# Optimization experiments

Hardware: AMD Instinct MI355X
Metric: run time of the kernel (lower is better)

## Reference

```python
import jax, jax.numpy as jnp
import numpy as np

B, T, H, W, C = 2, 8, 20, 36, 512
NH = 4
HD = C // NH
WS = (5, 9)
EXP = (2, 4)              # window_size // 2
KP = (5, 9)               # focal unfold kernel for level k=0
PADP = (2, 4)
T2T_K, T2T_S, T2T_P = (7, 7), (3, 3), (3, 3)
FFN_HD = 1960
NWH, NWW = H // WS[0], W // WS[1]   # 4, 4
WAREA = WS[0] * WS[1]               # 45


def _valid_ind_rolled():
    wh, ww = WS
    eh, ew = EXP
    m = np.ones((4, wh, ww), np.float32)
    m[0, :wh - eh, :ww - ew] = 0   # tl
    m[1, :wh - eh, ew:] = 0        # tr
    m[2, eh:, :ww - ew] = 0        # bl
    m[3, eh:, ew:] = 0             # br
    return jnp.asarray(np.nonzero(m.reshape(-1))[0])

VALID_ROLLED = _valid_ind_rolled()  # (120,)


def unfold(x, k, s, p):
    # x: (N, Cc, Hh, Ww) -> (N, Cc*kh*kw, L); matches torch.nn.Unfold layout (c slowest).
    N, Cc, Hh, Ww = x.shape
    kh, kw = k; sh, sw = s; ph, pw = p
    xp = jnp.pad(x, ((0, 0), (0, 0), (ph, ph), (pw, pw)))
    oh = (Hh + 2 * ph - kh) // sh + 1
    ow = (Ww + 2 * pw - kw) // sw + 1
    cols = [xp[:, :, i:i + oh * sh:sh, j:j + ow * sw:sw]
            for i in range(kh) for j in range(kw)]
    patches = jnp.stack(cols, axis=2)            # (N, Cc, kh*kw, oh, ow)
    return patches.reshape(N, Cc * kh * kw, oh * ow)


def fold(patches, out_hw, k, s, p):
    # inverse of unfold (overlap-add), matches torch F.fold.
    N = patches.shape[0]
    kh, kw = k; sh, sw = s; ph, pw = p
    Hh, Ww = out_hw
    oh = (Hh + 2 * ph - kh) // sh + 1
    ow = (Ww + 2 * pw - kw) // sw + 1
    Cc = patches.shape[1] // (kh * kw)
    pr = patches.reshape(N, Cc, kh, kw, oh, ow)
    out = jnp.zeros((N, Cc, Hh + 2 * ph, Ww + 2 * pw), patches.dtype)
    for i in range(kh):
        for j in range(kw):
            out = out.at[:, :, i:i + oh * sh:sh, j:j + ow * sw:sw].add(pr[:, :, i, j])
    return out[:, :, ph:ph + Hh, pw:pw + Ww]


def layer_norm(x, g, b):
    mu = jnp.mean(x, -1, keepdims=True)
    var = jnp.var(x, -1, keepdims=True)
    return (x - mu) * jax.lax.rsqrt(var + 1e-5) * g + b


def win_part(x):
    # (B,T,H,W,C) -> (B*nW, T*wh*ww, C)
    b = x.shape[0]
    x = x.reshape(b, T, NWH, WS[0], NWW, WS[1], C)
    return x.transpose(0, 2, 4, 1, 3, 5, 6).reshape(-1, T * WAREA, C)


def to_heads(w):
    return w.reshape(-1, T, WAREA, NH, HD).transpose(0, 3, 1, 2, 4).reshape(-1, NH, T * WAREA, HD)


def block_forward(x, g1, be1, wqkv, bqkv, wproj, bproj, wpool, bpool, g2, be2, w1, bf1, w2, bf2, out_h, out_w):
    shortcut = x
    xn = layer_norm(x, g1, be1)

    # ---- coarser (pooled) focal level, k=0 (focal_level=2) ----
    wnr = xn.reshape(B, T, NWH, WS[0], NWW, WS[1], C).transpose(0, 2, 4, 1, 3, 5, 6)
    wnr = wnr.reshape(B, NWH, NWW, T, WAREA, C)
    pooled = jnp.einsum('bhwtnc,n->bhwtc', wnr, wpool) + bpool   # (B,NWH,NWW,T,C)

    # ---- window attention ----
    qkv = xn @ wqkv + bqkv                                       # (B,T,H,W,3C)
    q, k, v = jnp.split(qkv, 3, axis=-1)
    qw = to_heads(win_part(q)) * (HD ** -0.5)
    kw_, vw = to_heads(win_part(k)), to_heads(win_part(v))

    def rolled(t):
        parts = []
        for sh, sw in ((-EXP[0], -EXP[1]), (-EXP[0], EXP[1]), (EXP[0], -EXP[1]), (EXP[0], EXP[1])):
            r = jnp.roll(t, (sh, sw), axis=(2, 3))
            parts.append(win_part(r).reshape(-1, T, WAREA, NH, HD))
        cat = jnp.concatenate(parts, axis=2)                     # (B*nW, T, 4*warea, NH, HD)
        cat = jnp.take(cat.transpose(0, 3, 1, 2, 4), VALID_ROLLED, axis=3)
        return cat.reshape(-1, NH, T * VALID_ROLLED.shape[0], HD)

    k_rolled = jnp.concatenate([kw_, rolled(k)], axis=2)         # (B*nW, NH, T*165, HD)
    v_rolled = jnp.concatenate([vw, rolled(v)], axis=2)

    # pooled keys/values via focal unfold
    xp = pooled.transpose(0, 3, 1, 2, 4)                          # (B,T,NWH,NWW,C)
    qkv_p = xp @ wqkv + bqkv
    kp, vp = qkv_p[..., C:2 * C], qkv_p[..., 2 * C:]

    def unfold_kv(t):
        t = t.transpose(0, 1, 4, 2, 3).reshape(B * T, C, NWH, NWW)
        u = unfold(t, KP, (1, 1), PADP)                           # (B*T, C*45, L)
        L = u.shape[-1]
        u = u.reshape(B, T, C, KP[0], KP[1], L).transpose(0, 5, 1, 3, 4, 2)
        u = u.reshape(B * L, T, KP[0] * KP[1], NH, HD).transpose(0, 3, 1, 2, 4)
        return u.reshape(B * L, NH, T * KP[0] * KP[1], HD)

    k_all = jnp.concatenate([k_rolled, unfold_kv(kp)], axis=2)
    v_all = jnp.concatenate([v_rolled, unfold_kv(vp)], axis=2)

    attn = jnp.einsum('wnqd,wnkd->wnqk', qw, k_all)               # (B*nW, NH, T*45, N)

    # validity mask for pooled context (zero-padded unfold positions -> -100)
    ones = jnp.ones((T, 1, NWH, NWW), x.dtype)
    um = unfold(ones, KP, (1, 1), PADP)                           # (T, 45, L)
    L = um.shape[-1]
    mvals = jnp.where(um.reshape(T, KP[0] * KP[1], L).transpose(2, 0, 1).reshape(L, -1) == 0,
                      jnp.asarray(-100.0, x.dtype), jnp.asarray(0.0, x.dtype))
    n_rolled = k_rolled.shape[2]
    mask_cols = jnp.concatenate([jnp.zeros((L, n_rolled), x.dtype), mvals], axis=1)
    attn = attn + jnp.tile(mask_cols, (B, 1))[:, None, None, :]

    attn = jax.nn.softmax(attn, axis=-1)
    out = jnp.einsum('wnqk,wnkd->wnqd', attn, v_all)
    out = out.transpose(0, 2, 1, 3).reshape(-1, T * WAREA, C) @ wproj + bproj

    # window reverse + residual
    out = out.reshape(B, NWH, NWW, T, WS[0], WS[1], C)
    out = out.transpose(0, 3, 1, 4, 2, 5, 6).reshape(B, T, H, W, C)
    x = shortcut + out

    # ---- FusionFeedForward (fold/unfold re-normalized MLP) ----
    y = layer_norm(x, g2, be2).reshape(B, T * H * W, C)
    h = y @ w1 + bf1                                              # (B, n, 1960)
    nvec = ((out_h + 2 * T2T_P[0] - T2T_K[0]) // T2T_S[0] + 1) * \
           ((out_w + 2 * T2T_P[1] - T2T_K[1]) // T2T_S[1] + 1)
    bt = (B * T * H * W) // nvec
    norm_p = jnp.ones((bt, T2T_K[0] * T2T_K[1], nvec), x.dtype)
    norm_f = fold(norm_p, (out_h, out_w), T2T_K, T2T_S, T2T_P)    # (bt,1,out_h,out_w)
    h_f = fold(h.reshape(bt, nvec, FFN_HD).transpose(0, 2, 1), (out_h, out_w), T2T_K, T2T_S, T2T_P)
    h = unfold(h_f / norm_f, T2T_K, T2T_S, T2T_P).transpose(0, 2, 1).reshape(B, T * H * W, FFN_HD)
    h = jax.nn.gelu(h, approximate=False) @ w2 + bf2
    return x + h.reshape(B, T, H, W, C)


def setup_inputs() -> dict:
    key = jax.random.key(0)
    ks = jax.random.split(key, 8)
    s = 0.02
    return dict(
        x=jax.random.normal(ks[0], (B, T, H, W, C), jnp.float32),
        g1=jnp.ones((C,), jnp.float32),
        be1=jnp.zeros((C,), jnp.float32),
        wqkv=jax.random.normal(ks[1], (C, 3 * C), jnp.float32) * s,
        bqkv=jnp.zeros((3 * C,), jnp.float32),
        wproj=jax.random.normal(ks[2], (C, C), jnp.float32) * s,
        bproj=jnp.zeros((C,), jnp.float32),
        wpool=jnp.full((WAREA,), 1.0 / WAREA, jnp.float32),
        bpool=jnp.zeros((1,), jnp.float32),
        g2=jnp.ones((C,), jnp.float32),
        be2=jnp.zeros((C,), jnp.float32),
        w1=jax.random.normal(ks[3], (C, FFN_HD), jnp.float32) * s,
        bf1=jnp.zeros((FFN_HD,), jnp.float32),
        w2=jax.random.normal(ks[4], (FFN_HD, C), jnp.float32) * s,
        bf2=jnp.zeros((C,), jnp.float32),
        out_h=60,
        out_w=108,
    )


def reference(x, g1, be1, wqkv, bqkv, wproj, bproj, wpool, bpool, g2, be2, w1, bf1, w2, bf2, out_h, out_w):
    return block_forward(x, g1, be1, wqkv, bqkv, wproj, bproj, wpool, bpool,
                         g2, be2, w1, bf1, w2, bf2, out_h, out_w)
```

## Files before the change

### kernel.cpp

```cpp
#include <hip/hip_runtime.h>
#include <hip/hip_bf16.h>
#include <math.h>

typedef __hip_bfloat16 bf16;
typedef __attribute__((ext_vector_type(8))) short bf16x8;
typedef __attribute__((ext_vector_type(4))) float f32x4;

#define DEVI __device__ __forceinline__

#define C_ 512
#define NH_ 4
#define NTOK 11520
#define NKEY 1680
#define NRK 120
#define FFN_ 1960
#define ZROW (NTOK + 256)

DEVI float ldf(const bf16* p) { return __bfloat162float(*p); }
DEVI float ldf(const float* p) { return *p; }
DEVI void stw(bf16* p, float v) { *p = __float2bfloat16(v); }
DEVI void stw(float* p, float v) { *p = v; }
DEVI unsigned short f2bs(float f) { bf16 h = __float2bfloat16(f); return *(unsigned short*)&h; }

template <int DT> DEVI float ldw(const void* p, size_t i) {
  if (DT == 0) return __bfloat162float(((const bf16*)p)[i]);
  else         return ((const float*)p)[i];
}

DEVI void gload_lds16(const void* g, void* l) {
  __builtin_amdgcn_global_load_lds(
      (const __attribute__((address_space(1))) void*)g,
      (__attribute__((address_space(3))) void*)l, 16, 0, 0);
}

__global__ void k_init(const void* __restrict__ g1, int* __restrict__ flag,
                       int* __restrict__ table, bf16* __restrict__ zp) {
  if (blockIdx.x == 0) {
    if (threadIdx.x == 0) {
      const unsigned short* p = (const unsigned short*)g1;
      *flag = (p[0] == 0x3F80u) ? 0 : 1;
      int cnt = 0;
      for (int pq = 0; pq < 4; pq++)
        for (int wi = 0; wi < 5; wi++)
          for (int wj = 0; wj < 9; wj++) {
            bool invalid;
            if (pq == 0)      invalid = (wi < 3) && (wj < 5);
            else if (pq == 1) invalid = (wi < 3) && (wj >= 4);
            else if (pq == 2) invalid = (wi >= 2) && (wj < 5);
            else              invalid = (wi >= 2) && (wj >= 4);
            if (!invalid) table[cnt++] = pq * 45 + wi * 9 + wj;
          }
    }
  } else {
    zp[(blockIdx.x - 1) * 256 + threadIdx.x] = __float2bfloat16(0.f);
  }
}

__global__ void k_ksrc(const int* __restrict__ vtab, int* __restrict__ ksrc) {
  int idx = blockIdx.x * 256 + threadIdx.x;
  if (idx >= 32 * NKEY) return;
  int w = idx / NKEY, j = idx % NKEY;
  int b = w >> 4, nh = (w >> 2) & 3, nw = w & 3;
  int val;
  if (j < 360) {
    int t = j / 45, pos = j % 45, wi = pos / 9, wj2 = pos % 9;
    val = ((b * 8 + t) * 20 + nh * 5 + wi) * 36 + nw * 9 + wj2;
  } else if (j < 1320) {
    int jj = j - 360;
    int t = jj / 120, r = jj % 120;
    int id = vtab[r];
    int p = id / 45, pos = id % 45, wi = pos / 9, wj2 = pos % 9;
    int sh = (p < 2) ? -2 : 2;
    int sw = (p & 1) ? 4 : -4;
    int hh = nh * 5 + wi - sh;
    if (hh < 0) hh += 20; else if (hh >= 20) hh -= 20;
    int ww2 = nw * 9 + wj2 - sw;
    if (ww2 < 0) ww2 += 36; else if (ww2 >= 36) ww2 -= 36;
    val = ((b * 8 + t) * 20 + hh) * 36 + ww2;
  } else {
    int jj = j - 1320;
    int t = jj / 45, kidx = jj % 45, ki = kidx / 9, kj = kidx % 9;
    int snh = nh + ki - 2, snw = nw + kj - 4;
    if (snh < 0 || snh >= 4 || snw < 0 || snw >= 4) val = -1;
    else val = NTOK + (b * 8 + t) * 16 + snh * 4 + snw;
  }
  ksrc[idx] = val;
}

template <int DT>
DEVI void wcvt_body(const void* in, bf16* out, int K, int N, int Npad) {
  __shared__ float t[64][65];
  const int n0 = blockIdx.x * 64;
  const int k0 = blockIdx.y * 64;
  const int tx = threadIdx.x & 63, tg = threadIdx.x >> 6;
#pragma unroll
  for (int r = 0; r < 16; r++) {
    int k = k0 + r * 4 + tg;
    int nn = n0 + tx;
    float v = (k < K && nn < N) ? ldw<DT>(in, (size_t)k * N + nn) : 0.f;
    t[r * 4 + tg][tx] = v;
  }
  __syncthreads();
#pragma unroll
  for (int r = 0; r < 16; r++) {
    int nn = n0 + r * 4 + tg;
    int k = k0 + tx;
    if (nn < Npad && k < K)
      out[(size_t)nn * K + k] = __float2bfloat16(t[tx][r * 4 + tg]);
  }
}
__global__ void k_wcvt(const int* __restrict__ dflag, const void* __restrict__ in,
                       bf16* __restrict__ out, int K, int N, int Npad) {
  if (*dflag == 0) wcvt_body<0>(in, out, K, N, Npad);
  else             wcvt_body<1>(in, out, K, N, Npad);
}

__global__ void k_bcvt4(const int* __restrict__ dflag,
                        const void* __restrict__ b0, float* __restrict__ o0,
                        const void* __restrict__ b1, float* __restrict__ o1,
                        const void* __restrict__ b2, float* __restrict__ o2,
                        const void* __restrict__ b3, float* __restrict__ o3) {
  int dt = *dflag;
  int bx = blockIdx.x;
  const void* src; float* dst; int n, i;
  if (bx < 6)       { src = b0; dst = o0; n = 1536; i = bx * 256 + threadIdx.x; }
  else if (bx < 8)  { src = b1; dst = o1; n = 512;  i = (bx - 6) * 256 + threadIdx.x; }
  else if (bx < 16) { src = b2; dst = o2; n = FFN_; i = (bx - 8) * 256 + threadIdx.x; }
  else              { src = b3; dst = o3; n = 512;  i = (bx - 16) * 256 + threadIdx.x; }
  if (i < n) dst[i] = (dt == 0) ? ldw<0>(src, i) : ldw<1>(src, i);
}

template <int DTIN, int DTP>
DEVI void ln_body(const void* xin, const void* g, const void* be, bf16* out) {
  const int tok = blockIdx.x;
  const int tid = threadIdx.x;
  const size_t base = (size_t)tok * C_;
  float v0 = ldw<DTIN>(xin, base + tid);
  float v1 = ldw<DTIN>(xin, base + tid + 256);
  float s = v0 + v1, ss = v0 * v0 + v1 * v1;
#pragma unroll
  for (int o = 32; o; o >>= 1) { s += __shfl_xor(s, o); ss += __shfl_xor(ss, o); }
  __shared__ float sh[10];
  const int lane = tid & 63, wv = tid >> 6;
  if (lane == 0) { sh[wv] = s; sh[4 + wv] = ss; }
  __syncthreads();
  if (tid == 0) {
    float a = sh[0] + sh[1] + sh[2] + sh[3];
    float q = sh[4] + sh[5] + sh[6] + sh[7];
    float mu = a * (1.0f / C_);
    float var = q * (1.0f / C_) - mu * mu;
    sh[8] = mu; sh[9] = rsqrtf(fmaxf(var, 0.f) + 1e-5f);
  }
  __syncthreads();
  float mu = sh[8], inv = sh[9];
  stw(out + base + tid,
      (v0 - mu) * inv * ldw<DTP>(g, tid) + ldw<DTP>(be, tid));
  stw(out + base + tid + 256,
      (v1 - mu) * inv * ldw<DTP>(g, tid + 256) + ldw<DTP>(be, tid + 256));
}
__global__ void k_ln(const int* __restrict__ dflag, int mode,
                     const void* __restrict__ xin, const void* __restrict__ g,
                     const void* __restrict__ be, bf16* __restrict__ out) {
  int dt = *dflag;
  if (mode == 0) {
    if (dt == 0) ln_body<0, 0>(xin, g, be, out);
    else         ln_body<1, 1>(xin, g, be, out);
  } else {
    if (dt == 0) ln_body<1, 0>(xin, g, be, out);
    else         ln_body<1, 1>(xin, g, be, out);
  }
}

template <int DT>
DEVI void pool_body(const bf16* xn, const void* wpool, const void* bpool,
                    float* pooled) {
  int idx = blockIdx.x * blockDim.x + threadIdx.x;
  if (idx >= 256 * C_) return;
  int c = idx & (C_ - 1);
  int fw = idx >> 9;
  int nw = fw & 3, nh = (fw >> 2) & 3;
  int bt = fw >> 4;
  float acc = ldw<DT>(bpool, 0);
  for (int wi = 0; wi < 5; wi++) {
    int hh = nh * 5 + wi;
    const bf16* base = xn + (((size_t)(bt * 20 + hh)) * 36 + nw * 9) * C_ + c;
    for (int wj = 0; wj < 9; wj++)
      acc += __bfloat162float(base[(size_t)wj * C_]) * ldw<DT>(wpool, wi * 9 + wj);
  }
  pooled[idx] = acc;
}
__global__ void k_pool(const int* __restrict__ dflag, const bf16* __restrict__ xn,
                       const void* __restrict__ wpool, const void* __restrict__ bpool,
                       float* __restrict__ pooled) {
  if (*dflag == 0) pool_body<0>(xn, wpool, bpool, pooled);
  else             pool_body<1>(xn, wpool, bpool, pooled);
}

template <int DT>
DEVI void gemm_small_body(const float* A, const void* Bw, const void* bias,
                          bf16* Cc) {
  __shared__ float As[8][512];
  const int n = blockIdx.x * 256 + threadIdx.x;
  const int m0 = blockIdx.y * 8;
  for (int i = threadIdx.x; i < 8 * 512; i += 256)
    As[i >> 9][i & 511] = A[(size_t)(m0 + (i >> 9)) * 512 + (i & 511)];
  __syncthreads();
  float acc[8];
  float bv = ldw<DT>(bias, n);
#pragma unroll
  for (int mm = 0; mm < 8; mm++) acc[mm] = bv;
  for (int k = 0; k < 512; k++) {
    float b = ldw<DT>(Bw, (size_t)k * 1536 + n);
#pragma unroll
    for (int mm = 0; mm < 8; mm++) acc[mm] += As[mm][k] * b;
  }
#pragma unroll
  for (int mm = 0; mm < 8; mm++)
    Cc[(size_t)(m0 + mm) * 1536 + n] = __float2bfloat16(acc[mm]);
}
__global__ void k_gemm_small(const int* __restrict__ dflag, const float* __restrict__ A,
                             const void* __restrict__ Bw, const void* __restrict__ bias,
                             bf16* __restrict__ Cc) {
  if (*dflag == 0) gemm_small_body<0>(A, Bw, bias, Cc);
  else             gemm_small_body<1>(A, Bw, bias, Cc);
}

template <int RES>
__global__ __launch_bounds__(256) void k_gemm_m(const int* __restrict__ dflag,
                                                const bf16* __restrict__ A,
                                                const bf16* __restrict__ Bt,
                                                const float* __restrict__ bias,
                                                const void* __restrict__ resid,
                                                void* __restrict__ out,
                                                int M, int N, int K) {
  const int dt = dflag ? *dflag : 0;
  __shared__ __align__(16) unsigned short As[2][128 * 32];
  __shared__ __align__(16) unsigned short Bs[2][128 * 32];
  const int tid = threadIdx.x;
  const int lane = tid & 63, wid = tid >> 6;
  const int r15 = lane & 15, quad = lane >> 4;
  const int wm = wid >> 1, wn = wid & 1;
  const int nbx = gridDim.x;
  const int lin = blockIdx.x + nbx * blockIdx.y;
  const int cpx = (nbx * gridDim.y) >> 3;
  const int swz = (lin & 7) * cpx + (lin >> 3);
  const int m0 = (swz / nbx) * 128, n0 = (swz % nbx) * 128;

  f32x4 acc[4][4];
#pragma unroll
  for (int i = 0; i < 4; i++)
#pragma unroll
    for (int j = 0; j < 4; j++)
#pragma unroll
      for (int e = 0; e < 4; e++) acc[i][j][e] = 0.f;

  const int lrow = lane >> 2, lcol = (lane & 3) * 8;

  for (int k0 = 0; k0 < K; k0 += 64) {
    int rem = K - k0;
    if (rem >= 64) {
      const bf16* ga = A + (size_t)(m0 + wid * 32 + lrow) * K + k0 + lcol;
      gload_lds16(ga, &As[0][wid * 1024]);
      gload_lds16(ga + (size_t)16 * K, &As[0][wid * 1024 + 512]);
      gload_lds16(ga + 32, &As[1][wid * 1024]);
      gload_lds16(ga + (size_t)16 * K + 32, &As[1][wid * 1024 + 512]);
      const bf16* gb = Bt + (size_t)(n0 + wid * 32 + lrow) * K + k0 + lcol;
      gload_lds16(gb, &Bs[0][wid * 1024]);
      gload_lds16(gb + (size_t)16 * K, &Bs[0][wid * 1024 + 512]);
      gload_lds16(gb + 32, &Bs[1][wid * 1024]);
      gload_lds16(gb + (size_t)16 * K + 32, &Bs[1][wid * 1024 + 512]);
    } else {
      int r = tid >> 3, c = (tid & 7) * 8;
      uint4 z = make_uint4(0, 0, 0, 0);
      int h = c >> 5, cc = c & 31;
#pragma unroll
      for (int p = 0; p < 4; p++) {
        int row = r + p * 32;
        uint4 av = z, bv = z;
        if (c < rem) {
          av = *(const uint4*)(A + (size_t)(m0 + row) * K + k0 + c);
          bv = *(const uint4*)(Bt + (size_t)(n0 + row) * K + k0 + c);
        }
        *(uint4*)&As[h][row * 32 + cc] = av;
        *(uint4*)&Bs[h][row * 32 + cc] = bv;
      }
    }
    __syncthreads();

#pragma unroll
    for (int h = 0; h < 2; h++) {
      bf16x8 af[4], bfr[4];
#pragma unroll
      for (int mf = 0; mf < 4; mf++)
        af[mf] = *(const bf16x8*)&As[h][(wm * 64 + mf * 16 + r15) * 32 + quad * 8];
#pragma unroll
      for (int nf = 0; nf < 4; nf++)
        bfr[nf] = *(const bf16x8*)&Bs[h][(wn * 64 + nf * 16 + r15) * 32 + quad * 8];
#pragma unroll
      for (int mf = 0; mf < 4; mf++)
#pragma unroll
        for (int nf = 0; nf < 4; nf++)
          acc[mf][nf] = __builtin_amdgcn_mfma_f32_16x16x32_bf16(af[mf], bfr[nf],
                                                                acc[mf][nf], 0, 0, 0);
    }
    __syncthreads();
  }

#pragma unroll
  for (int nf = 0; nf < 4; nf++) {
    int n = n0 + wn * 64 + nf * 16 + r15;
    if (n >= N) continue;
    float bv = bias[n];
#pragma unroll
    for (int mf = 0; mf < 4; mf++) {
      int mb = m0 + wm * 64 + mf * 16 + quad * 4;
#pragma unroll
      for (int e = 0; e < 4; e++) {
        size_t off = (size_t)(mb + e) * N + n;
        float v = acc[mf][nf][e] + bv;
        if (RES == 1) v += (dt == 0) ? ldw<0>(resid, off) : ldw<1>(resid, off);
        else if (RES == 2) v += ((const float*)resid)[off];
        if (RES == 0) ((bf16*)out)[off] = __float2bfloat16(v);
        else if (RES == 1) ((float*)out)[off] = v;
        else {
          if (dt == 0) ((bf16*)out)[off] = __float2bfloat16(v);
          else         ((float*)out)[off] = v;
        }
      }
    }
  }
}

#define KT 64
#define KPAD 136
#define VPAD 72
__global__ __launch_bounds__(768) void k_attn_m(const bf16* __restrict__ qkv,
                                                const int* __restrict__ ksrc,
                                                bf16* __restrict__ ao) {
  __shared__ int ks_l[NKEY];
  __shared__ __align__(16) unsigned short ktl[2][KT * KPAD];
  __shared__ __align__(16) unsigned short vtl[2][128 * VPAD];
  __shared__ __align__(16) unsigned short ptl[12 * 16 * VPAD];
  __shared__ float maskv[2][KT];

  const int tid = threadIdx.x;
  const int lane = tid & 63, wid = tid >> 6;
  const int r15 = lane & 15, quad = lane >> 4;
  const int w = blockIdx.x, qt = blockIdx.y, n = blockIdx.z;
  const int b = w >> 4, nh = (w >> 2) & 3, nw = w & 3;
  const unsigned short* qkvs = (const unsigned short*)qkv;

  for (int j = tid; j < NKEY; j += 768) ks_l[j] = ksrc[w * NKEY + j];

  bf16x8 qf[4];
  {
    int qw = qt * 192 + wid * 16 + r15;
    int qc2 = qw < 360 ? qw : 359;
    int t = qc2 / 45, pos = qc2 % 45, wi = pos / 9, wj = pos % 9;
    int tok = ((b * 8 + t) * 20 + nh * 5 + wi) * 36 + nw * 9 + wj;
    const unsigned short* qp = qkvs + (size_t)tok * 1536 + n * 128 + quad * 8;
#pragma unroll
    for (int c = 0; c < 4; c++)
      qf[c] = *(const bf16x8*)(qp + c * 32);
  }

  f32x4 of[8];
#pragma unroll
  for (int nt = 0; nt < 8; nt++)
#pragma unroll
    for (int e = 0; e < 4; e++) of[nt][e] = 0.f;
  float m_[4], l_[4];
#pragma unroll
  for (int e = 0; e < 4; e++) { m_[e] = -1e30f; l_[e] = 0.f; }

  unsigned short* ptw = &ptl[wid * 16 * VPAD];

  const bool isK = (wid < 4);
  const int kr = tid >> 2, kp = tid & 3;
  const int vr = lane, vp8 = wid - 4;
  uint4 k0, k1, k2, k3, v0, v1;
  float mreg = -30000.f;
  const unsigned short* kbase = qkvs + 512 + n * 128 + kp * 32;
  const unsigned short* vbase = qkvs + 1024 + n * 128 + vp8 * 16;

  auto load_tile = [&](int j0) {
    int cnt = NKEY - j0; if (cnt > KT) cnt = KT;
    if (isK) {
      int s0 = (kr < cnt) ? ks_l[j0 + kr] : -1;
      mreg = (s0 < 0) ? -30000.f : 0.f;
      int row = (s0 < 0) ? ZROW : s0;
      const uint4* kq = (const uint4*)(kbase + (size_t)row * 1536);
      k0 = kq[0]; k1 = kq[1]; k2 = kq[2]; k3 = kq[3];
    } else {
      int s1 = (vr < cnt) ? ks_l[j0 + vr] : -1;
      int row = (s1 < 0) ? ZROW : s1;
      const uint4* vq = (const uint4*)(vbase + (size_t)row * 1536);
      v0 = vq[0]; v1 = vq[1];
    }
  };

  auto store_tile = [&](int buf) {
    if (isK) {
      if (kp == 0) maskv[buf][kr] = mreg;
      unsigned short* kb = &ktl[buf][kr * KPAD + kp * 32];
      *(uint4*)&kb[0]  = k0;
      *(uint4*)&kb[8]  = k1;
      *(uint4*)&kb[16] = k2;
      *(uint4*)&kb[24] = k3;
    } else {
      unsigned short* vb = &vtl[buf][0];
      int d0 = vp8 * 16;
      vb[(d0 + 0) * VPAD + vr]  = (unsigned short)(v0.x & 0xFFFFu);
      vb[(d0 + 1) * VPAD + vr]  = (unsigned short)(v0.x >> 16);
      vb[(d0 + 2) * VPAD + vr]  = (unsigned short)(v0.y & 0xFFFFu);
      vb[(d0 + 3) * VPAD + vr]  = (unsigned short)(v0.y >> 16);
      vb[(d0 + 4) * VPAD + vr]  = (unsigned short)(v0.z & 0xFFFFu);
      vb[(d0 + 5) * VPAD + vr]  = (unsigned short)(v0.z >> 16);
      vb[(d0 + 6) * VPAD + vr]  = (unsigned short)(v0.w & 0xFFFFu);
      vb[(d0 + 7) * VPAD + vr]  = (unsigned short)(v0.w >> 16);
      vb[(d0 + 8) * VPAD + vr]  = (unsigned short)(v1.x & 0xFFFFu);
      vb[(d0 + 9) * VPAD + vr]  = (unsigned short)(v1.x >> 16);
      vb[(d0 + 10) * VPAD + vr] = (unsigned short)(v1.y & 0xFFFFu);
      vb[(d0 + 11) * VPAD + vr] = (unsigned short)(v1.y >> 16);
      vb[(d0 + 12) * VPAD + vr] = (unsigned short)(v1.z & 0xFFFFu);
      vb[(d0 + 13) * VPAD + vr] = (unsigned short)(v1.z >> 16);
      vb[(d0 + 14) * VPAD + vr] = (unsigned short)(v1.w & 0xFFFFu);
      vb[(d0 + 15) * VPAD + vr] = (unsigned short)(v1.w >> 16);
    }
  };

  __syncthreads();
  load_tile(0);
  store_tile(0);
  load_tile(KT);
  __syncthreads();

  int cur = 0, j0 = 0;
  while (true) {
    int nxt = j0 + KT;
    if (nxt < NKEY) {
      store_tile(cur ^ 1);
      if (nxt + KT < NKEY) load_tile(nxt + KT);
    }

    const unsigned short* ktc = &ktl[cur][0];
    const unsigned short* vtc = &vtl[cur][0];
    const float* mkc = maskv[cur];

    f32x4 sf[4];
#pragma unroll
    for (int ft = 0; ft < 4; ft++)
#pragma unroll
      for (int e = 0; e < 4; e++) sf[ft][e] = 0.f;
#pragma unroll
    for (int kc = 0; kc < 4; kc++) {
      bf16x8 a = qf[kc];
#pragma unroll
      for (int ft = 0; ft < 4; ft++) {
        bf16x8 bb = *(const bf16x8*)&ktc[(ft * 16 + r15) * KPAD + kc * 32 + quad * 8];
        sf[ft] = __builtin_amdgcn_mfma_f32_16x16x32_bf16(a, bb, sf[ft], 0, 0, 0);
      }
    }
    const float scl = 0.088388347648318447f;
#pragma unroll
    for (int ft = 0; ft < 4; ft++) {
      float mk = mkc[ft * 16 + r15];
#pragma unroll
      for (int e = 0; e < 4; e++) sf[ft][e] = sf[ft][e] * scl + mk;
    }
    float tm[4];
#pragma unroll
    for (int e = 0; e < 4; e++) {
      float v = fmaxf(fmaxf(sf[0][e], sf[1][e]), fmaxf(sf[2][e], sf[3][e]));
#pragma unroll
      for (int o = 1; o < 16; o <<= 1) v = fmaxf(v, __shfl_xor(v, o));
      tm[e] = v;
    }
    bool grow = (tm[0] > m_[0] + 8.f) | (tm[1] > m_[1] + 8.f) |
                (tm[2] > m_[2] + 8.f) | (tm[3] > m_[3] + 8.f);
    if (__any(grow)) {
#pragma unroll
      for (int e = 0; e < 4; e++) {
        float mn = fmaxf(m_[e], tm[e]);
        float alpha = __expf(m_[e] - mn);
        m_[e] = mn;
        float rs = 0.f;
#pragma unroll
        for (int ft = 0; ft < 4; ft++) {
          float pv = __expf(sf[ft][e] - mn);
          rs += pv;
          ptw[(quad * 4 + e) * VPAD + ft * 16 + r15] = f2bs(pv);
        }
        l_[e] = l_[e] * alpha + rs;
#pragma unroll
        for (int nt = 0; nt < 8; nt++) of[nt][e] *= alpha;
      }
    } else {
#pragma unroll
      for (int e = 0; e < 4; e++) {
        float rs = 0.f;
#pragma unroll
        for (int ft = 0; ft < 4; ft++) {
          float pv = __expf(sf[ft][e] - m_[e]);
          rs += pv;
          ptw[(quad * 4 + e) * VPAD + ft * 16 + r15] = f2bs(pv);
        }
        l_[e] += rs;
      }
    }
#pragma unroll
    for (int kc = 0; kc < 2; kc++) {
      bf16x8 pa = *(const bf16x8*)&ptw[r15 * VPAD + kc * 32 + quad * 8];
#pragma unroll
      for (int nt = 0; nt < 8; nt++) {
        bf16x8 vb = *(const bf16x8*)&vtc[(nt * 16 + r15) * VPAD + kc * 32 + quad * 8];
        of[nt] = __builtin_amdgcn_mfma_f32_16x16x32_bf16(pa, vb, of[nt], 0, 0, 0);
      }
    }

    if (nxt >= NKEY) break;
    __syncthreads();
    cur ^= 1; j0 = nxt;
  }

#pragma unroll
  for (int e = 0; e < 4; e++) {
#pragma unroll
    for (int o = 1; o < 16; o <<= 1) l_[e] += __shfl_xor(l_[e], o);
  }
#pragma unroll
  for (int e = 0; e < 4; e++) {
    int qw = qt * 192 + wid * 16 + quad * 4 + e;
    if (qw >= 360) continue;
    float inv = 1.0f / l_[e];
    int t = qw / 45, pos = qw % 45, wi = pos / 9, wj = pos % 9;
    int tok = ((b * 8 + t) * 20 + nh * 5 + wi) * 36 + nw * 9 + wj;
    bf16* op = ao + (size_t)tok * 512 + n * 128 + r15;
#pragma unroll
    for (int nt = 0; nt < 8; nt++)
      stw(op + nt * 16, of[nt][e] * inv);
  }
}

__global__ void k_fold(const bf16* __restrict__ h1, float* __restrict__ hf) {
  int idx = blockIdx.x * 256 + threadIdx.x;
  if (idx >= 16 * 40 * 60 * 108) return;
  int x = idx % 108;
  int tmp = idx / 108;
  int y = tmp % 60; tmp /= 60;
  int c = tmp % 40;
  int bt = tmp / 40;
  float sum = 0.f;
  int cnt = 0;
  for (int ki = y % 3; ki < 7; ki += 3) {
    int num = y + 3 - ki;
    if (num < 0) continue;
    int oh = num / 3;
    if (oh >= 20) continue;
    for (int kj = x % 3; kj < 7; kj += 3) {
      int num2 = x + 3 - kj;
      if (num2 < 0) continue;
      int ow = num2 / 3;
      if (ow >= 36) continue;
      sum += __bfloat162float(
          h1[(size_t)(bt * 720 + oh * 36 + ow) * FFN_ + c * 49 + ki * 7 + kj]);
      cnt++;
    }
  }
  hf[idx] = sum / (float)cnt;
}

__global__ void k_unfold_gelu(const float* __restrict__ hf, bf16* __restrict__ h2) {
  int idx = blockIdx.x * 256 + threadIdx.x;
  if (idx >= NTOK * FFN_) return;
  int f = idx % FFN_;
  int token = idx / FFN_;
  int c = f / 49, k = f % 49, ki = k / 7, kj = k % 7;
  int bt = token / 720, vec = token % 720;
  int oh = vec / 36, ow = vec % 36;
  int y = oh * 3 + ki - 3, x = ow * 3 + kj - 3;
  float v = 0.f;
  if (y >= 0 && y < 60 && x >= 0 && x < 108)
    v = hf[((size_t)(bt * 40 + c) * 60 + y) * 108 + x];
  float g = 0.5f * v * (1.0f + erff(v * 0.70710678118654752f));
  stw(h2 + idx, g);
}

extern "C" void kernel_launch(void* const* d_in, const int* in_sizes, int n_in,
                              void* d_out, int out_size, void* d_ws, size_t ws_size,
                              hipStream_t stream) {
  (void)in_sizes; (void)n_in; (void)out_size; (void)ws_size;
  const void* x     = d_in[0];
  const void* g1    = d_in[1];
  const void* be1   = d_in[2];
  const void* wqkv  = d_in[3];
  const void* bqkv  = d_in[4];
  const void* wproj = d_in[5];
  const void* bproj = d_in[6];
  const void* wpool = d_in[7];
  const void* bpool = d_in[8];
  const void* g2    = d_in[9];
  const void* be2   = d_in[10];
  const void* w1    = d_in[11];
  const void* bf1   = d_in[12];
  const void* w2    = d_in[13];
  const void* bf2   = d_in[14];

  char* ws = (char*)d_ws;
  size_t off = 0;
  auto alloc = [&](size_t bytes) -> void* {
    void* p = ws + off;
    off += (bytes + 255) & ~(size_t)255;
    return p;
  };

  int*   dflag  = (int*)  alloc(256);
  int*   vtab   = (int*)  alloc(NRK * sizeof(int));
  int*   ksrc   = (int*)  alloc((size_t)32 * NKEY * sizeof(int));
  bf16*  buf2   = (bf16*) alloc((size_t)NTOK * FFN_ * 2);
  float* pooled = (float*)alloc((size_t)256 * C_ * 4);
  float* x2     = (float*)alloc((size_t)NTOK * C_ * 4);
  float* hf     = (float*)alloc((size_t)16 * 40 * 60 * 108 * 4);
  bf16*  wqkv_t = (bf16*) alloc((size_t)1536 * 512 * 2);
  bf16*  wproj_t= (bf16*) alloc((size_t)512 * 512 * 2);
  bf16*  w1_t   = (bf16*) alloc((size_t)2048 * 512 * 2);
  bf16*  w2_t   = (bf16*) alloc((size_t)512 * FFN_ * 2);
  float* bqkv_f = (float*)alloc(1536 * 4);
  float* bproj_f= (float*)alloc(512 * 4);
  float* bf1_f  = (float*)alloc(FFN_ * 4);
  float* bf2_f  = (float*)alloc(512 * 4);

  bf16* buf1 = (bf16*)d_out;
  bf16* xn = buf1;
  bf16* ao = buf1;
  bf16* y  = buf1;
  bf16* qkv = buf2;
  bf16* h1  = buf2;
  bf16* qkvpb = buf2 + (size_t)NTOK * 1536;

  k_init<<<7, 256, 0, stream>>>(g1, dflag, vtab, qkvpb + (size_t)256 * 1536);
  k_ksrc<<<(32 * NKEY) / 256, 256, 0, stream>>>(vtab, ksrc);

  k_wcvt<<<dim3(24, 8), 256, 0, stream>>>(dflag, wqkv, wqkv_t, 512, 1536, 1536);
  k_wcvt<<<dim3(8, 8), 256, 0, stream>>>(dflag, wproj, wproj_t, 512, 512, 512);
  k_wcvt<<<dim3(32, 8), 256, 0, stream>>>(dflag, w1, w1_t, 512, FFN_, 2048);
  k_wcvt<<<dim3(8, 31), 256, 0, stream>>>(dflag, w2, w2_t, FFN_, 512, 512);
  k_bcvt4<<<18, 256, 0, stream>>>(dflag, bqkv, bqkv_f, bproj, bproj_f,
                                  bf1, bf1_f, bf2, bf2_f);

  k_ln<<<NTOK, 256, 0, stream>>>(dflag, 0, x, g1, be1, xn);

  k_pool<<<512, 256, 0, stream>>>(dflag, xn, wpool, bpool, pooled);

  k_gemm_m<0><<<dim3(12, 90), 256, 0, stream>>>(
      nullptr, xn, wqkv_t, bqkv_f, nullptr, qkv, NTOK, 1536, 512);

  k_gemm_small<<<dim3(6, 32), 256, 0, stream>>>(dflag, pooled, wqkv, bqkv, qkvpb);

  k_attn_m<<<dim3(32, 2, NH_), 768, 0, stream>>>(qkv, ksrc, ao);

  k_gemm_m<1><<<dim3(4, 90), 256, 0, stream>>>(
      dflag, ao, wproj_t, bproj_f, x, x2, NTOK, 512, 512);

  k_ln<<<NTOK, 256, 0, stream>>>(dflag, 1, x2, g2, be2, y);

  k_gemm_m<0><<<dim3(16, 90), 256, 0, stream>>>(
      nullptr, y, w1_t, bf1_f, nullptr, h1, NTOK, FFN_, 512);

  k_fold<<<(16 * 40 * 60 * 108) / 256, 256, 0, stream>>>(h1, hf);

  k_unfold_gelu<<<(NTOK * FFN_) / 256, 256, 0, stream>>>(hf, h1);

  k_gemm_m<2><<<dim3(4, 90), 256, 0, stream>>>(
      dflag, h1, w2_t, bf2_f, x2, d_out, NTOK, 512, FFN_);
}
```

Before: 542.9 us.

## Enlarge GEMM tiles to 256 rows, batch weight conversion, move GELU into fold

The main GEMM now runs 512-thread workgroups over 256x128 output tiles with a remainder-aware XCD swizzle. The goal is better reuse of B-tile loads and fewer workgroups. The four weight-transpose launches are merged into one kernel. GELU is applied once per folded pixel inside the fold kernel, which now writes a bf16 intermediate, so the unfold pass becomes a plain gather of half-size data instead of recomputing erf for every patch element. This rounds the pre-unfold activations to bf16 a step earlier and doubles LDS per block, which may reduce occupancy.

```diff
diff --git a/kernel.cpp b/kernel.cpp
--- a/kernel.cpp
+++ b/kernel.cpp
@@ -88,10 +88,9 @@
 }
 
 template <int DT>
-DEVI void wcvt_body(const void* in, bf16* out, int K, int N, int Npad) {
+DEVI void wcvt_body(const void* in, bf16* out, int K, int N, int Npad,
+                    int n0, int k0) {
   __shared__ float t[64][65];
-  const int n0 = blockIdx.x * 64;
-  const int k0 = blockIdx.y * 64;
   const int tx = threadIdx.x & 63, tg = threadIdx.x >> 6;
 #pragma unroll
   for (int r = 0; r < 16; r++) {
@@ -109,10 +108,20 @@
       out[(size_t)nn * K + k] = __float2bfloat16(t[tx][r * 4 + tg]);
   }
 }
-__global__ void k_wcvt(const int* __restrict__ dflag, const void* __restrict__ in,
-                       bf16* __restrict__ out, int K, int N, int Npad) {
-  if (*dflag == 0) wcvt_body<0>(in, out, K, N, Npad);
-  else             wcvt_body<1>(in, out, K, N, Npad);
+__global__ void k_wcvt4(const int* __restrict__ dflag,
+                        const void* __restrict__ i0, bf16* __restrict__ o0,
+                        const void* __restrict__ i1, bf16* __restrict__ o1,
+                        const void* __restrict__ i2, bf16* __restrict__ o2,
+                        const void* __restrict__ i3, bf16* __restrict__ o3) {
+  int b = blockIdx.x;
+  const void* in; bf16* out; int K, N, Npad, nb, lb;
+  if (b < 192)      { in = i0; out = o0; K = 512;  N = 1536; Npad = 1536; nb = 24; lb = b; }
+  else if (b < 256) { in = i1; out = o1; K = 512;  N = 512;  Npad = 512;  nb = 8;  lb = b - 192; }
+  else if (b < 512) { in = i2; out = o2; K = 512;  N = FFN_; Npad = 2048; nb = 32; lb = b - 256; }
+  else              { in = i3; out = o3; K = FFN_; N = 512;  Npad = 512;  nb = 8;  lb = b - 512; }
+  int n0 = (lb % nb) * 64, k0 = (lb / nb) * 64;
+  if (*dflag == 0) wcvt_body<0>(in, out, K, N, Npad, n0, k0);
+  else             wcvt_body<1>(in, out, K, N, Npad, n0, k0);
 }
 
 __global__ void k_bcvt4(const int* __restrict__ dflag,
@@ -226,25 +235,27 @@
 }
 
 template <int RES>
-__global__ __launch_bounds__(256) void k_gemm_m(const int* __restrict__ dflag,
-                                                const bf16* __restrict__ A,
-                                                const bf16* __restrict__ Bt,
-                                                const float* __restrict__ bias,
-                                                const void* __restrict__ resid,
-                                                void* __restrict__ out,
-                                                int M, int N, int K) {
+__global__ __launch_bounds__(512) void k_gemm_m2(const int* __restrict__ dflag,
+                                                 const bf16* __restrict__ A,
+                                                 const bf16* __restrict__ Bt,
+                                                 const float* __restrict__ bias,
+                                                 const void* __restrict__ resid,
+                                                 void* __restrict__ out,
+                                                 int M, int N, int K) {
   const int dt = dflag ? *dflag : 0;
-  __shared__ __align__(16) unsigned short As[2][128 * 32];
+  __shared__ __align__(16) unsigned short As[2][256 * 32];
   __shared__ __align__(16) unsigned short Bs[2][128 * 32];
   const int tid = threadIdx.x;
   const int lane = tid & 63, wid = tid >> 6;
   const int r15 = lane & 15, quad = lane >> 4;
   const int wm = wid >> 1, wn = wid & 1;
   const int nbx = gridDim.x;
+  const int nwg = nbx * gridDim.y;
   const int lin = blockIdx.x + nbx * blockIdx.y;
-  const int cpx = (nbx * gridDim.y) >> 3;
-  const int swz = (lin & 7) * cpx + (lin >> 3);
-  const int m0 = (swz / nbx) * 128, n0 = (swz % nbx) * 128;
+  const int q8 = nwg >> 3, r8 = nwg & 7;
+  const int xcd = lin & 7, ii = lin >> 3;
+  const int swz = (xcd < r8 ? xcd * (q8 + 1) : r8 * (q8 + 1) + (xcd - r8) * q8) + ii;
+  const int m0 = (swz / nbx) * 256, n0 = (swz % nbx) * 128;
 
   f32x4 acc[4][4];
 #pragma unroll
@@ -264,24 +275,25 @@
       gload_lds16(ga + (size_t)16 * K, &As[0][wid * 1024 + 512]);
       gload_lds16(ga + 32, &As[1][wid * 1024]);
       gload_lds16(ga + (size_t)16 * K + 32, &As[1][wid * 1024 + 512]);
-      const bf16* gb = Bt + (size_t)(n0 + wid * 32 + lrow) * K + k0 + lcol;
-      gload_lds16(gb, &Bs[0][wid * 1024]);
-      gload_lds16(gb + (size_t)16 * K, &Bs[0][wid * 1024 + 512]);
-      gload_lds16(gb + 32, &Bs[1][wid * 1024]);
-      gload_lds16(gb + (size_t)16 * K + 32, &Bs[1][wid * 1024 + 512]);
+      const bf16* gb = Bt + (size_t)(n0 + wid * 16 + lrow) * K + k0 + lcol;
+      gload_lds16(gb, &Bs[0][wid * 512]);
+      gload_lds16(gb + 32, &Bs[1][wid * 512]);
     } else {
       int r = tid >> 3, c = (tid & 7) * 8;
       uint4 z = make_uint4(0, 0, 0, 0);
       int h = c >> 5, cc = c & 31;
 #pragma unroll
       for (int p = 0; p < 4; p++) {
-        int row = r + p * 32;
-        uint4 av = z, bv = z;
-        if (c < rem) {
-          av = *(const uint4*)(A + (size_t)(m0 + row) * K + k0 + c);
-          bv = *(const uint4*)(Bt + (size_t)(n0 + row) * K + k0 + c);
-        }
+        int row = r + p * 64;
+        uint4 av = z;
+        if (c < rem) av = *(const uint4*)(A + (size_t)(m0 + row) * K + k0 + c);
         *(uint4*)&As[h][row * 32 + cc] = av;
+      }
+#pragma unroll
+      for (int p = 0; p < 2; p++) {
+        int row = r + p * 64;
+        uint4 bv = z;
+        if (c < rem) bv = *(const uint4*)(Bt + (size_t)(n0 + row) * K + k0 + c);
         *(uint4*)&Bs[h][row * 32 + cc] = bv;
       }
     }
@@ -542,7 +554,7 @@
   }
 }
 
-__global__ void k_fold(const bf16* __restrict__ h1, float* __restrict__ hf) {
+__global__ void k_fold(const bf16* __restrict__ h1, bf16* __restrict__ hg) {
   int idx = blockIdx.x * 256 + threadIdx.x;
   if (idx >= 16 * 40 * 60 * 108) return;
   int x = idx % 108;
@@ -567,10 +579,12 @@
       cnt++;
     }
   }
-  hf[idx] = sum / (float)cnt;
-}
-
-__global__ void k_unfold_gelu(const float* __restrict__ hf, bf16* __restrict__ h2) {
+  float v = sum / (float)cnt;
+  float g = 0.5f * v * (1.0f + erff(v * 0.70710678118654752f));
+  hg[idx] = __float2bfloat16(g);
+}
+
+__global__ void k_unfold_gelu(const bf16* __restrict__ hg, bf16* __restrict__ h2) {
   int idx = blockIdx.x * 256 + threadIdx.x;
   if (idx >= NTOK * FFN_) return;
   int f = idx % FFN_;
@@ -579,11 +593,10 @@
   int bt = token / 720, vec = token % 720;
   int oh = vec / 36, ow = vec % 36;
   int y = oh * 3 + ki - 3, x = ow * 3 + kj - 3;
-  float v = 0.f;
+  bf16 g = __float2bfloat16(0.f);
   if (y >= 0 && y < 60 && x >= 0 && x < 108)
-    v = hf[((size_t)(bt * 40 + c) * 60 + y) * 108 + x];
-  float g = 0.5f * v * (1.0f + erff(v * 0.70710678118654752f));
-  stw(h2 + idx, g);
+    g = hg[((size_t)(bt * 40 + c) * 60 + y) * 108 + x];
+  h2[idx] = g;
 }
 
 extern "C" void kernel_launch(void* const* d_in, const int* in_sizes, int n_in,
@@ -620,7 +633,7 @@
   bf16*  buf2   = (bf16*) alloc((size_t)NTOK * FFN_ * 2);
   float* pooled = (float*)alloc((size_t)256 * C_ * 4);
   float* x2     = (float*)alloc((size_t)NTOK * C_ * 4);
-  float* hf     = (float*)alloc((size_t)16 * 40 * 60 * 108 * 4);
+  bf16*  hg     = (bf16*) alloc((size_t)16 * 40 * 60 * 108 * 2);
   bf16*  wqkv_t = (bf16*) alloc((size_t)1536 * 512 * 2);
   bf16*  wproj_t= (bf16*) alloc((size_t)512 * 512 * 2);
   bf16*  w1_t   = (bf16*) alloc((size_t)2048 * 512 * 2);
@@ -641,10 +654,8 @@
   k_init<<<7, 256, 0, stream>>>(g1, dflag, vtab, qkvpb + (size_t)256 * 1536);
   k_ksrc<<<(32 * NKEY) / 256, 256, 0, stream>>>(vtab, ksrc);
 
-  k_wcvt<<<dim3(24, 8), 256, 0, stream>>>(dflag, wqkv, wqkv_t, 512, 1536, 1536);
-  k_wcvt<<<dim3(8, 8), 256, 0, stream>>>(dflag, wproj, wproj_t, 512, 512, 512);
-  k_wcvt<<<dim3(32, 8), 256, 0, stream>>>(dflag, w1, w1_t, 512, FFN_, 2048);
-  k_wcvt<<<dim3(8, 31), 256, 0, stream>>>(dflag, w2, w2_t, FFN_, 512, 512);
+  k_wcvt4<<<760, 256, 0, stream>>>(dflag, wqkv, wqkv_t, wproj, wproj_t,
+                                   w1, w1_t, w2, w2_t);
   k_bcvt4<<<18, 256, 0, stream>>>(dflag, bqkv, bqkv_f, bproj, bproj_f,
                                   bf1, bf1_f, bf2, bf2_f);
 
@@ -652,25 +663,25 @@
 
   k_pool<<<512, 256, 0, stream>>>(dflag, xn, wpool, bpool, pooled);
 
-  k_gemm_m<0><<<dim3(12, 90), 256, 0, stream>>>(
+  k_gemm_m2<0><<<dim3(12, 45), 512, 0, stream>>>(
       nullptr, xn, wqkv_t, bqkv_f, nullptr, qkv, NTOK, 1536, 512);
 
   k_gemm_small<<<dim3(6, 32), 256, 0, stream>>>(dflag, pooled, wqkv, bqkv, qkvpb);
 
   k_attn_m<<<dim3(32, 2, NH_), 768, 0, stream>>>(qkv, ksrc, ao);
 
-  k_gemm_m<1><<<dim3(4, 90), 256, 0, stream>>>(
+  k_gemm_m2<1><<<dim3(4, 45), 512, 0, stream>>>(
       dflag, ao, wproj_t, bproj_f, x, x2, NTOK, 512, 512);
 
   k_ln<<<NTOK, 256, 0, stream>>>(dflag, 1, x2, g2, be2, y);
 
-  k_gemm_m<0><<<dim3(16, 90), 256, 0, stream>>>(
+  k_gemm_m2<0><<<dim3(16, 45), 512, 0, stream>>>(
       nullptr, y, w1_t, bf1_f, nullptr, h1, NTOK, FFN_, 512);
 
-  k_fold<<<(16 * 40 * 60 * 108) / 256, 256, 0, stream>>>(h1, hf);
-
-  k_unfold_gelu<<<(NTOK * FFN_) / 256, 256, 0, stream>>>(hf, h1);
-
-  k_gemm_m<2><<<dim3(4, 90), 256, 0, stream>>>(
+  k_fold<<<(16 * 40 * 60 * 108) / 256, 256, 0, stream>>>(h1, hg);
+
+  k_unfold_gelu<<<(NTOK * FFN_) / 256, 256, 0, stream>>>(hg, h1);
+
+  k_gemm_m2<2><<<dim3(4, 45), 512, 0, stream>>>(
       dflag, h1, w2_t, bf2_f, x2, d_out, NTOK, 512, FFN_);
 }
```

Measured after the change: 573.7 us. 1.06x slower.
